# Kernel tuning notes

Measured on AMD Instinct MI355X. Metric: run time of the kernel, lower is better.

The kernel has to match this reference:

```python
import jax, jax.numpy as jnp
import numpy as np

N, E, G = 50000, 800000, 128      # nodes, edges, graphs
IN, H, OUT = 128, 128, 2          # feature dims
K, L = 3, 3                       # Chebyshev order, num conv layers
EPS = 1e-5


def setup_inputs() -> dict:
    key = jax.random.key(0)
    ks = jax.random.split(key, 10)
    x = jax.random.normal(ks[0], (N, IN), dtype=jnp.float32)
    edge_index = jax.random.randint(ks[1], (2, E), 0, N, dtype=jnp.int64)
    batch = jnp.sort(jax.random.randint(ks[2], (N,), 0, G, dtype=jnp.int64))
    w_in = jax.random.normal(ks[3], (IN, H), dtype=jnp.float32) * 0.05
    b_in = jnp.zeros((H,), jnp.float32)
    ln_g = jnp.ones((H,), jnp.float32)
    ln_b = jnp.zeros((H,), jnp.float32)
    cheb_w = jax.random.normal(ks[4], (L, K, H, H), dtype=jnp.float32) * 0.05
    cheb_b = jnp.zeros((L, H), jnp.float32)
    bn_g = jnp.ones((L, H), jnp.float32)
    bn_b = jnp.zeros((L, H), jnp.float32)
    w1 = jax.random.normal(ks[5], (H, H // 2), dtype=jnp.float32) * 0.05
    b1 = jnp.zeros((H // 2,), jnp.float32)
    w2 = jax.random.normal(ks[6], (H // 2, OUT), dtype=jnp.float32) * 0.05
    b2 = jnp.zeros((OUT,), jnp.float32)
    return dict(x=x, w_in=w_in, b_in=b_in, ln_g=ln_g, ln_b=ln_b,
                cheb_w=cheb_w, cheb_b=cheb_b, bn_g=bn_g, bn_b=bn_b,
                w1=w1, b1=b1, w2=w2, b2=b2,
                edge_index=edge_index, batch=batch)


def reference(x, w_in, b_in, ln_g, ln_b, cheb_w, cheb_b, bn_g, bn_b,
              w1, b1, w2, b2, edge_index, batch):
    src, dst = edge_index[0], edge_index[1]

    # ChebConv scaled Laplacian with lambda_max=2, sym norm:
    # L_hat = -D^{-1/2} A D^{-1/2}  (self-loop terms cancel in PyG's __norm__)
    deg = jax.ops.segment_sum(jnp.ones((E,), x.dtype), src, num_segments=N)
    dinv = jnp.where(deg > 0, jax.lax.rsqrt(jnp.maximum(deg, 1.0)), 0.0)
    w_edge = -dinv[src] * dinv[dst]  # [E]

    def spmm(h):  # y_i = sum_{(j->i)} w_edge * h_j
        return jax.ops.segment_sum(w_edge[:, None] * h[src], dst, num_segments=N)

    # node_embed: Linear -> LayerNorm -> ReLU (dropout p used in eval => identity)
    h = x @ w_in + b_in
    mu = h.mean(-1, keepdims=True)
    var = h.var(-1, keepdims=True)
    h = (h - mu) * jax.lax.rsqrt(var + EPS) * ln_g + ln_b
    h = jax.nn.relu(h)

    hiddens = [h]
    for l in range(L):
        # Chebyshev recurrence: T0 = h, T1 = L_hat h, Tk = 2 L_hat T_{k-1} - T_{k-2}
        tx0 = h
        out = tx0 @ cheb_w[l, 0]
        tx1 = spmm(tx0)
        out = out + tx1 @ cheb_w[l, 1]
        for k in range(2, K):
            tx2 = 2.0 * spmm(tx1) - tx0
            out = out + tx2 @ cheb_w[l, k]
            tx0, tx1 = tx1, tx2
        out = out + cheb_b[l]
        # BatchNorm1d over nodes (training-mode batch statistics, biased var)
        m = out.mean(0)
        v = out.var(0)
        out = (out - m) * jax.lax.rsqrt(v + EPS) * bn_g[l] + bn_b[l]
        h = jax.nn.relu(out)
        hiddens.append(h)

    # Laplacian (Dirichlet) regularization over all hidden states
    reg = jnp.float32(0.0)
    for hh in hiddens:
        diff = hh[src] - hh[dst]              # [E, H]
        reg = reg + jnp.mean(jnp.sum(diff * diff, axis=-1))
    reg = reg / len(hiddens)

    # global mean pool over batch assignment
    counts = jax.ops.segment_sum(jnp.ones((N,), x.dtype), batch, num_segments=G)
    gsum = jax.ops.segment_sum(h, batch, num_segments=G)
    gmean = gsum / jnp.maximum(counts, 1.0)[:, None]

    z = jax.nn.relu(gmean @ w1 + b1)
    logits = z @ w2 + b2
    return logits, reg
```

## Files before the change

### kernel.cpp

```cpp
#include <hip/hip_runtime.h>
#include <hip/hip_bf16.h>

#define NNODES 50000
#define NEDGES 800000
#define NGRAPH 128
#define CAP 64
#define EPSV 1e-5f

typedef __attribute__((ext_vector_type(8))) short bf16x8;
typedef __attribute__((ext_vector_type(8))) unsigned short us16x8;
typedef __attribute__((ext_vector_type(4))) float f32x4;
typedef __attribute__((ext_vector_type(2))) float f32x2;

__device__ __forceinline__ unsigned short f2bf(float f) {
    unsigned u = __float_as_uint(f);
    return (unsigned short)((u + 0x7fffu + ((u >> 16) & 1u)) >> 16);
}
__device__ __forceinline__ float bf2f(unsigned short h) {
    return __uint_as_float(((unsigned)h) << 16);
}
__device__ __forceinline__ unsigned pk4_fp8(float a, float b, float c, float d) {
    int w = __builtin_amdgcn_cvt_pk_fp8_f32(a, b, 0, false);
    w = __builtin_amdgcn_cvt_pk_fp8_f32(c, d, w, true);
    return (unsigned)w;
}

__global__ void fillA_kernel(const int* __restrict__ src, const int* __restrict__ dst,
                             int* __restrict__ outdeg, int* __restrict__ indeg,
                             unsigned* __restrict__ slot, int E) {
    int e = blockIdx.x * blockDim.x + threadIdx.x;
    if (e < E) {
        int s = src[e];
        int d = dst[e];
        atomicAdd(&outdeg[s], 1);
        int pos = atomicAdd(&indeg[d], 1);
        if (pos < CAP) slot[(size_t)d * CAP + pos] = (unsigned)s;
    }
}

__global__ void dinv_gstart_kernel(const int* __restrict__ outdeg, float* __restrict__ dinv,
                                   const int* __restrict__ batch, int* __restrict__ gstart, int n) {
    int i = blockIdx.x * blockDim.x + threadIdx.x;
    if (i < n) {
        int d = outdeg[i];
        dinv[i] = (d > 0) ? rsqrtf((float)d) : 0.0f;
    }
    if (blockIdx.x == 0 && threadIdx.x <= NGRAPH) {
        int g = threadIdx.x;
        int lo = 0, hi = n;
        while (lo < hi) {
            int mid = (lo + hi) >> 1;
            if (batch[mid] < g) lo = mid + 1; else hi = mid;
        }
        gstart[g] = lo;
    }
}

__global__ void pack_kernel(unsigned* __restrict__ slot, const int* __restrict__ indeg,
                            const float* __restrict__ dinv, int total) {
    int i = blockIdx.x * blockDim.x + threadIdx.x;
    if (i >= total) return;
    int node = i >> 6, k = i & (CAP - 1);
    int cnt = min(indeg[node], CAP);
    if (k < cnt) {
        unsigned idx = slot[i];
        slot[i] = idx | ((unsigned)f2bf(dinv[idx]) << 16);
    }
}

__global__ void wprep_kernel(const float* __restrict__ w_in, const float* __restrict__ cheb_w,
                             unsigned short* __restrict__ Wsp) {
    int p = blockIdx.x;
    int t = threadIdx.x;
    for (int s8 = 0; s8 < 8; ++s8) {
        int slot = s8 * 256 + t;
        int kc = slot >> 9, ct = (slot >> 6) & 7, lane = slot & 63;
        int q = lane >> 4, nn = lane & 15;
        unsigned short* o = Wsp + ((size_t)p * 2048 + slot) * 16;
#pragma unroll
        for (int j = 0; j < 8; ++j) {
            int k = kc * 32 + q * 8 + j, c = ct * 16 + nn;
            float v;
            if (p == 0) {
                v = w_in[k * 128 + c];
            } else {
                int pl = (p - 1) / 3, kk = (p - 1) % 3;
                v = cheb_w[((size_t)(pl * 3 + kk) * 128 + k) * 128 + c];
                if (kk == 0) v -= cheb_w[((size_t)(pl * 3 + 2) * 128 + k) * 128 + c];
                else if (kk == 2) v *= 2.f;
            }
            unsigned short hi = f2bf(v);
            o[j] = hi;
            o[8 + j] = f2bf(v - bf2f(hi));
        }
    }
}

template <int NPARTS, int EPI, int AF32>
__global__ __launch_bounds__(256) void gemm_mfma(
    const void* __restrict__ A0v, const void* __restrict__ A1v, const void* __restrict__ A2v,
    const unsigned short* __restrict__ Wsp, const float* __restrict__ bias,
    unsigned short* __restrict__ out16,
    const float* __restrict__ g0, const float* __restrict__ b0,
    float* __restrict__ colsum, float* __restrict__ colsumsq, int n) {
    __shared__ float red[256];
    int t = threadIdx.x, w = t >> 6, l = t & 63;
    int m = l & 15, qk = l >> 4;
    int rowA = blockIdx.x * 64 + w * 16 + m;
    red[t] = 0.f;
    __syncthreads();

    f32x4 acc[8];
#pragma unroll
    for (int ct = 0; ct < 8; ++ct) acc[ct] = (f32x4){0.f, 0.f, 0.f, 0.f};

    bool valid = rowA < n;
#pragma unroll
    for (int p = 0; p < NPARTS; ++p) {
#pragma unroll
        for (int kc = 0; kc < 4; ++kc) {
            bf16x8 ah, al;
            if (AF32) {
                const float* arow = (const float*)A0v;
                if (p == 1) arow = (const float*)A1v;
                if (p == 2) arow = (const float*)A2v;
                arow += (size_t)rowA * 128;
                float4 x0, x1;
                if (valid) {
                    x0 = *(const float4*)&arow[kc * 32 + qk * 8];
                    x1 = *(const float4*)&arow[kc * 32 + qk * 8 + 4];
                } else {
                    x0 = make_float4(0.f, 0.f, 0.f, 0.f); x1 = x0;
                }
                float xs[8] = {x0.x, x0.y, x0.z, x0.w, x1.x, x1.y, x1.z, x1.w};
#pragma unroll
                for (int j = 0; j < 8; ++j) {
                    unsigned short hi = f2bf(xs[j]);
                    ah[j] = (short)hi;
                    al[j] = (short)f2bf(xs[j] - bf2f(hi));
                }
            } else {
                const unsigned short* arow = (const unsigned short*)A0v;
                if (p == 1) arow = (const unsigned short*)A1v;
                if (p == 2) arow = (const unsigned short*)A2v;
                arow += (size_t)rowA * 128;
                if (valid) ah = *(const bf16x8*)&arow[kc * 32 + qk * 8];
                else ah = (bf16x8){0, 0, 0, 0, 0, 0, 0, 0};
            }
            const unsigned short* wb = Wsp + ((size_t)((p * 4 + kc) * 8) * 64 + l) * 16;
#pragma unroll
            for (int ct = 0; ct < 8; ++ct) {
                bf16x8 bh = *(const bf16x8*)(wb + (size_t)ct * 64 * 16);
                bf16x8 bl = *(const bf16x8*)(wb + (size_t)ct * 64 * 16 + 8);
                acc[ct] = __builtin_amdgcn_mfma_f32_16x16x32_bf16(ah, bh, acc[ct], 0, 0, 0);
                if (AF32)
                    acc[ct] = __builtin_amdgcn_mfma_f32_16x16x32_bf16(al, bh, acc[ct], 0, 0, 0);
                acc[ct] = __builtin_amdgcn_mfma_f32_16x16x32_bf16(ah, bl, acc[ct], 0, 0, 0);
            }
        }
    }

    int rowC0 = blockIdx.x * 64 + w * 16 + qk * 4;
    if (EPI == 0) {
        float rs[4] = {0.f, 0.f, 0.f, 0.f}, rss[4] = {0.f, 0.f, 0.f, 0.f};
#pragma unroll
        for (int ct = 0; ct < 8; ++ct) {
            float b = bias[ct * 16 + m];
#pragma unroll
            for (int j = 0; j < 4; ++j) {
                float v = acc[ct][j] + b;
                acc[ct][j] = v;
                rs[j] += v; rss[j] += v * v;
            }
        }
#pragma unroll
        for (int off = 1; off < 16; off <<= 1) {
#pragma unroll
            for (int j = 0; j < 4; ++j) {
                rs[j] += __shfl_xor(rs[j], off, 64);
                rss[j] += __shfl_xor(rss[j], off, 64);
            }
        }
        float mean[4], rstd[4];
#pragma unroll
        for (int j = 0; j < 4; ++j) {
            mean[j] = rs[j] * (1.f / 128.f);
            float var = rss[j] * (1.f / 128.f) - mean[j] * mean[j];
            rstd[j] = rsqrtf(var + EPSV);
        }
#pragma unroll
        for (int ct = 0; ct < 8; ++ct) {
            int c = ct * 16 + m;
            float gg = g0[c], bb = b0[c];
#pragma unroll
            for (int j = 0; j < 4; ++j) {
                int gr = rowC0 + j;
                if (gr < n) {
                    float x = (acc[ct][j] - mean[j]) * rstd[j] * gg + bb;
                    x = fmaxf(x, 0.f);
                    out16[(size_t)gr * 128 + c] = f2bf(x);
                }
            }
        }
    } else {
#pragma unroll
        for (int ct = 0; ct < 8; ++ct) {
            int c = ct * 16 + m;
            float b = bias[c];
            float s = 0.f, ss = 0.f;
#pragma unroll
            for (int j = 0; j < 4; ++j) {
                int gr = rowC0 + j;
                if (gr < n) {
                    float v = acc[ct][j] + b;
                    out16[(size_t)gr * 128 + c] = f2bf(v);
                    s += v; ss += v * v;
                }
            }
            s += __shfl_xor(s, 16, 64);  ss += __shfl_xor(ss, 16, 64);
            s += __shfl_xor(s, 32, 64);  ss += __shfl_xor(ss, 32, 64);
            if (qk == 0) {
                atomicAdd(&red[c], s);
                atomicAdd(&red[128 + c], ss);
            }
        }
        __syncthreads();
        if (t < 128) {
            atomicAdd(&colsum[t], red[t]);
            atomicAdd(&colsumsq[t], red[128 + t]);
        }
    }
}

__global__ void repack8_kernel(const unsigned short* __restrict__ h16,
                               unsigned char* __restrict__ h8, int total8) {
    int i = blockIdx.x * blockDim.x + threadIdx.x;
    if (i >= total8) return;
    us16x8 a = ((const us16x8*)h16)[i];
    uint2 o;
    o.x = pk4_fp8(bf2f(a[0]), bf2f(a[1]), bf2f(a[2]), bf2f(a[3]));
    o.y = pk4_fp8(bf2f(a[4]), bf2f(a[5]), bf2f(a[6]), bf2f(a[7]));
    ((uint2*)h8)[i] = o;
}

template <int MODE>
__global__ void spmm_g(const unsigned char* __restrict__ g8,
                       const unsigned short* __restrict__ self16,
                       unsigned short* __restrict__ dst16, unsigned char* __restrict__ dst8,
                       const unsigned* __restrict__ slot,
                       const float* __restrict__ dinv,
                       const int* __restrict__ outdeg, const int* __restrict__ indeg,
                       int n, double* __restrict__ norm_slots, double* __restrict__ cross_slots) {
    int lane = threadIdx.x & 63;
    int g = lane >> 4;
    int q = lane & 15;
    int w = (int)((blockIdx.x * (unsigned)blockDim.x + threadIdx.x) >> 6) * 4 + g;
    bool active = w < n;
    int cnt = active ? min(indeg[w], CAP) : 0;
    size_t rbase = (size_t)w * 128 + q * 8;
    float hi[8];
    if (MODE != 1) {
#pragma unroll
        for (int j = 0; j < 8; ++j) hi[j] = 0.f;
        if (active) {
            us16x8 a = *(const us16x8*)&self16[rbase];
#pragma unroll
            for (int j = 0; j < 8; ++j) hi[j] = bf2f(a[j]);
        }
    }
    float acc[8];
#pragma unroll
    for (int j = 0; j < 8; ++j) acc[j] = 0.f;
    float cr = 0.f;
    size_t sbase = (size_t)w * CAP;
#pragma unroll
    for (int c = 0; c < 4; ++c) {
        if (c * 16 >= cnt) break;
        unsigned cw = (c * 16 + q < cnt) ? slot[sbase + c * 16 + q] : 0u;
        int mycnt = min(cnt - c * 16, 16);
        uint2 uu[16];
        float dd[16];
#pragma unroll
        for (int u = 0; u < 16; ++u) {
            unsigned cwu = __shfl(cw, (g << 4) + u, 64);
            int j = (int)(cwu & 0xFFFFu);
            dd[u] = bf2f((unsigned short)(cwu >> 16));
            uu[u] = make_uint2(0, 0);
            if (u < mycnt) uu[u] = *(const uint2*)&g8[(size_t)j * 128 + q * 8];
        }
#pragma unroll
        for (int u = 0; u < 16; ++u) {
            f32x2 l0 = __builtin_amdgcn_cvt_pk_f32_fp8(uu[u].x, false);
            f32x2 h0 = __builtin_amdgcn_cvt_pk_f32_fp8(uu[u].x, true);
            f32x2 l1 = __builtin_amdgcn_cvt_pk_f32_fp8(uu[u].y, false);
            f32x2 h1 = __builtin_amdgcn_cvt_pk_f32_fp8(uu[u].y, true);
            float v[8] = {l0.x, l0.y, h0.x, h0.y, l1.x, l1.y, h1.x, h1.y};
            if (MODE != 2) {
#pragma unroll
                for (int j = 0; j < 8; ++j) acc[j] += dd[u] * v[j];
            }
            if (MODE != 1) {
#pragma unroll
                for (int j = 0; j < 8; ++j) cr += hi[j] * v[j];
            }
        }
    }
    if (MODE != 2 && active) {
        float di = dinv[w];
        float v[8];
        us16x8 o;
#pragma unroll
        for (int j = 0; j < 8; ++j) { v[j] = -di * acc[j]; o[j] = f2bf(v[j]); }
        *(us16x8*)&dst16[rbase] = o;
        if (MODE == 0) {
            uint2 o8;
            o8.x = pk4_fp8(v[0], v[1], v[2], v[3]);
            o8.y = pk4_fp8(v[4], v[5], v[6], v[7]);
            *(uint2*)&dst8[(size_t)w * 128 + q * 8] = o8;
        }
    }
    if (MODE != 1) {
        float nt = 0.f;
#pragma unroll
        for (int j = 0; j < 8; ++j) nt += hi[j] * hi[j];
#pragma unroll
        for (int off = 8; off > 0; off >>= 1) {
            cr += __shfl_down(cr, off, 16);
            nt += __shfl_down(nt, off, 16);
        }
        if (q == 0 && active) {
            int slotid = w & 255;
            atomicAdd(&cross_slots[slotid], (double)cr);
            atomicAdd(&norm_slots[slotid], (double)nt * (double)(outdeg[w] + indeg[w]));
        }
    }
}

__global__ void bnrelu_kernel(const unsigned short* __restrict__ ob16,
                              const float* __restrict__ colsum, const float* __restrict__ colsumsq,
                              const float* __restrict__ bn_g, const float* __restrict__ bn_b,
                              unsigned short* __restrict__ h16, unsigned char* __restrict__ h8,
                              int n, int total4) {
    __shared__ float ssc[128], ssh[128];
    int t = threadIdx.x;
    if (t < 128) {
        float m = colsum[t] / (float)n;
        float v = colsumsq[t] / (float)n - m * m;
        float sc = bn_g[t] * rsqrtf(v + EPSV);
        ssc[t] = sc;
        ssh[t] = bn_b[t] - m * sc;
    }
    __syncthreads();
    int i = blockIdx.x * blockDim.x + t;
    if (i >= total4) return;
    ushort4 o = ((const ushort4*)ob16)[i];
    int c = (i * 4) & 127;
    float4 r;
    r.x = fmaxf(bf2f(o.x) * ssc[c + 0] + ssh[c + 0], 0.f);
    r.y = fmaxf(bf2f(o.y) * ssc[c + 1] + ssh[c + 1], 0.f);
    r.z = fmaxf(bf2f(o.z) * ssc[c + 2] + ssh[c + 2], 0.f);
    r.w = fmaxf(bf2f(o.w) * ssc[c + 3] + ssh[c + 3], 0.f);
    ushort4 u = make_ushort4(f2bf(r.x), f2bf(r.y), f2bf(r.z), f2bf(r.w));
    ((ushort4*)h16)[i] = u;
    ((unsigned*)h8)[i] = pk4_fp8(r.x, r.y, r.z, r.w);
}

__global__ void poolmlp_kernel(const unsigned short* __restrict__ h16, const int* __restrict__ start,
                               const float* __restrict__ w1, const float* __restrict__ b1,
                               const float* __restrict__ w2, const float* __restrict__ b2,
                               const double* __restrict__ norm_slots,
                               const double* __restrict__ cross_slots,
                               float* __restrict__ out) {
    __shared__ float sm[2][128];
    __shared__ float gm[128];
    int g = blockIdx.x, t = threadIdx.x;
    int half = t >> 7, c = t & 127;
    int s = start[g], e = start[g + 1];
    float acc = 0.f;
    for (int r = s + half; r < e; r += 2) acc += bf2f(h16[(size_t)r * 128 + c]);
    sm[half][c] = acc;
    __syncthreads();
    if (t < 128) {
        float cnt = fmaxf((float)(e - s), 1.f);
        gm[t] = (sm[0][t] + sm[1][t]) / cnt;
    }
    __syncthreads();
    if (t < 64) {
        float z = b1[t];
        for (int k = 0; k < 128; ++k) z += gm[k] * w1[(size_t)k * 64 + t];
        z = fmaxf(z, 0.f);
        float p0 = z * w2[t * 2 + 0];
        float p1 = z * w2[t * 2 + 1];
        for (int off = 32; off > 0; off >>= 1) {
            p0 += __shfl_down(p0, off, 64);
            p1 += __shfl_down(p1, off, 64);
        }
        if (t == 0) {
            out[g * 2 + 0] = p0 + b2[0];
            out[g * 2 + 1] = p1 + b2[1];
        }
    } else if (g == 0 && t < 128) {
        int l = t - 64;
        double ns = 0.0, cs = 0.0;
        for (int i = l; i < 256; i += 64) { ns += norm_slots[i]; cs += cross_slots[i]; }
        for (int off = 32; off > 0; off >>= 1) {
            ns += __shfl_down(ns, off, 64);
            cs += __shfl_down(cs, off, 64);
        }
        if (l == 0) out[256] = (float)((ns - 2.0 * cs) / ((double)NEDGES * 4.0));
    }
}

extern "C" void kernel_launch(void* const* d_in, const int* in_sizes, int n_in,
                              void* d_out, int out_size, void* d_ws, size_t ws_size,
                              hipStream_t stream) {
    const float* x      = (const float*)d_in[0];
    const float* w_in   = (const float*)d_in[1];
    const float* b_in   = (const float*)d_in[2];
    const float* ln_g   = (const float*)d_in[3];
    const float* ln_b   = (const float*)d_in[4];
    const float* cheb_w = (const float*)d_in[5];
    const float* cheb_b = (const float*)d_in[6];
    const float* bn_g   = (const float*)d_in[7];
    const float* bn_b   = (const float*)d_in[8];
    const float* w1     = (const float*)d_in[9];
    const float* b1     = (const float*)d_in[10];
    const float* w2     = (const float*)d_in[11];
    const float* b2     = (const float*)d_in[12];
    const int*   eidx   = (const int*)d_in[13];
    const int*   batch  = (const int*)d_in[14];
    const int* src = eidx;
    const int* dst = eidx + NEDGES;
    float* out = (float*)d_out;

    char* ws = (char*)d_ws;
    size_t off = 0;
    auto alloc = [&](size_t bytes) -> void* {
        void* p = ws + off;
        off = (off + bytes + 255) & ~(size_t)255;
        return p;
    };
    unsigned short* ob16 = (unsigned short*)alloc((size_t)NNODES * 128 * 2);
    unsigned short* h16  = (unsigned short*)alloc((size_t)NNODES * 128 * 2);
    unsigned short* t116 = (unsigned short*)alloc((size_t)NNODES * 128 * 2);
    unsigned short* s16  = (unsigned short*)alloc((size_t)NNODES * 128 * 2);
    unsigned char*  h8   = (unsigned char*)alloc((size_t)NNODES * 128);
    unsigned char*  t18  = (unsigned char*)alloc((size_t)NNODES * 128);
    unsigned short* Wsp  = (unsigned short*)alloc((size_t)10 * 2048 * 16 * 2);
    int* degs     = (int*)alloc((size_t)2 * NNODES * 4);
    int* outdeg   = degs;
    int* indeg    = degs + NNODES;
    float* dinv   = (float*)alloc((size_t)NNODES * 4);
    unsigned* slot = (unsigned*)alloc((size_t)NNODES * CAP * 4);
    int* gstart   = (int*)alloc((size_t)(NGRAPH + 1) * 4);
    float* colstats = (float*)alloc(768 * 4 + 512 * 8);
    double* dslots  = (double*)(colstats + 768);
    double* norm_slots  = dslots;
    double* cross_slots = dslots + 256;

    hipMemsetAsync(degs, 0, (size_t)2 * NNODES * 4, stream);
    hipMemsetAsync(colstats, 0, 768 * 4 + 512 * 8, stream);

    int tE = (NEDGES + 255) / 256;
    int tN = (NNODES + 255) / 256;
    fillA_kernel<<<tE, 256, 0, stream>>>(src, dst, outdeg, indeg, slot, NEDGES);
    dinv_gstart_kernel<<<tN, 256, 0, stream>>>(outdeg, dinv, batch, gstart, NNODES);
    pack_kernel<<<(NNODES * CAP + 255) / 256, 256, 0, stream>>>(slot, indeg, dinv, NNODES * CAP);
    wprep_kernel<<<10, 256, 0, stream>>>(w_in, cheb_w, Wsp);

    int gemmBlocks = (NNODES + 63) / 64;
    int nodes4 = (NNODES + 3) / 4;
    int spmmBlocks = (nodes4 * 64 + 255) / 256;
    int total4 = NNODES * 128 / 4;
    int total8 = NNODES * 128 / 8;

    gemm_mfma<1, 0, 1><<<gemmBlocks, 256, 0, stream>>>(x, nullptr, nullptr, Wsp, b_in, h16,
                                                       ln_g, ln_b, nullptr, nullptr, NNODES);
    repack8_kernel<<<(total8 + 255) / 256, 256, 0, stream>>>(h16, h8, total8);

    for (int l = 0; l < 3; ++l) {
        float* colsum = colstats + 256 * l;
        float* colsumsq = colsum + 128;
        spmm_g<0><<<spmmBlocks, 256, 0, stream>>>(h8, h16, t116, t18, slot, dinv,
                                                  outdeg, indeg, NNODES, norm_slots, cross_slots);
        spmm_g<1><<<spmmBlocks, 256, 0, stream>>>(t18, nullptr, s16, nullptr, slot, dinv,
                                                  outdeg, indeg, NNODES, nullptr, nullptr);
        gemm_mfma<3, 1, 0><<<gemmBlocks, 256, 0, stream>>>(h16, t116, s16,
            Wsp + (size_t)(1 + 3 * l) * 2048 * 16, cheb_b + (size_t)l * 128, ob16,
            nullptr, nullptr, colsum, colsumsq, NNODES);
        bnrelu_kernel<<<(total4 + 255) / 256, 256, 0, stream>>>(ob16, colsum, colsumsq,
            bn_g + (size_t)l * 128, bn_b + (size_t)l * 128, h16, h8, NNODES, total4);
    }
    spmm_g<2><<<spmmBlocks, 256, 0, stream>>>(h8, h16, nullptr, nullptr, slot, dinv,
                                              outdeg, indeg, NNODES, norm_slots, cross_slots);

    poolmlp_kernel<<<NGRAPH, 256, 0, stream>>>(h16, gstart, w1, b1, w2, b2,
                                               norm_slots, cross_slots, out);
}
```

Baseline: 695.8 us.

## Stage GEMM weights in LDS with register prefetch and fold dinv kernel into pack

The MFMA GEMM now copies each part's split-bf16 weight tile into shared memory, prefetching the next part's weights into registers while computing. All A-operand rows are loaded up front instead of inside the loop. Separately, the standalone dinv/gstart kernel and its dinv buffer are removed: pack and spmm compute rsqrt(outdeg) inline, saving one launch and one array. The LDS footprint grows to 64 KB per block, which can lower occupancy, and the extra barriers plus the larger register set add cost of their own.

```diff
diff --git a/kernel.cpp b/kernel.cpp
--- a/kernel.cpp
+++ b/kernel.cpp
@@ -38,13 +38,10 @@
     }
 }
 
-__global__ void dinv_gstart_kernel(const int* __restrict__ outdeg, float* __restrict__ dinv,
-                                   const int* __restrict__ batch, int* __restrict__ gstart, int n) {
-    int i = blockIdx.x * blockDim.x + threadIdx.x;
-    if (i < n) {
-        int d = outdeg[i];
-        dinv[i] = (d > 0) ? rsqrtf((float)d) : 0.0f;
-    }
+__global__ void pack_kernel(unsigned* __restrict__ slot, const int* __restrict__ indeg,
+                            const int* __restrict__ outdeg,
+                            const int* __restrict__ batch, int* __restrict__ gstart,
+                            int total, int n) {
     if (blockIdx.x == 0 && threadIdx.x <= NGRAPH) {
         int g = threadIdx.x;
         int lo = 0, hi = n;
@@ -54,17 +51,15 @@
         }
         gstart[g] = lo;
     }
-}
-
-__global__ void pack_kernel(unsigned* __restrict__ slot, const int* __restrict__ indeg,
-                            const float* __restrict__ dinv, int total) {
     int i = blockIdx.x * blockDim.x + threadIdx.x;
     if (i >= total) return;
     int node = i >> 6, k = i & (CAP - 1);
     int cnt = min(indeg[node], CAP);
     if (k < cnt) {
         unsigned idx = slot[i];
-        slot[i] = idx | ((unsigned)f2bf(dinv[idx]) << 16);
+        int d = outdeg[idx];
+        float dv = (d > 0) ? rsqrtf((float)d) : 0.0f;
+        slot[i] = idx | ((unsigned)f2bf(dv) << 16);
     }
 }
 
@@ -103,36 +98,79 @@
     unsigned short* __restrict__ out16,
     const float* __restrict__ g0, const float* __restrict__ b0,
     float* __restrict__ colsum, float* __restrict__ colsumsq, int n) {
-    __shared__ float red[256];
+    __shared__ unsigned short lds_hi[2048 * 8];
+    __shared__ unsigned short lds_lo[2048 * 8];
     int t = threadIdx.x, w = t >> 6, l = t & 63;
     int m = l & 15, qk = l >> 4;
     int rowA = blockIdx.x * 64 + w * 16 + m;
-    red[t] = 0.f;
-    __syncthreads();
+    bool valid = rowA < n;
 
     f32x4 acc[8];
 #pragma unroll
     for (int ct = 0; ct < 8; ++ct) acc[ct] = (f32x4){0.f, 0.f, 0.f, 0.f};
 
-    bool valid = rowA < n;
+    uint4 aB[NPARTS][4];
+    float4 aF[4][2];
+    if (AF32) {
+        const float* arow = (const float*)A0v + (size_t)rowA * 128;
+#pragma unroll
+        for (int kc = 0; kc < 4; ++kc) {
+            if (valid) {
+                aF[kc][0] = *(const float4*)&arow[kc * 32 + qk * 8];
+                aF[kc][1] = *(const float4*)&arow[kc * 32 + qk * 8 + 4];
+            } else {
+                aF[kc][0] = make_float4(0.f, 0.f, 0.f, 0.f);
+                aF[kc][1] = aF[kc][0];
+            }
+        }
+    } else {
+#pragma unroll
+        for (int p = 0; p < NPARTS; ++p) {
+            const unsigned short* arow = (const unsigned short*)A0v;
+            if (p == 1) arow = (const unsigned short*)A1v;
+            if (p == 2) arow = (const unsigned short*)A2v;
+            arow += (size_t)rowA * 128;
+#pragma unroll
+            for (int kc = 0; kc < 4; ++kc) {
+                if (valid) aB[p][kc] = *(const uint4*)&arow[kc * 32 + qk * 8];
+                else aB[p][kc] = make_uint4(0, 0, 0, 0);
+            }
+        }
+    }
+
+    const uint4* gw0 = (const uint4*)Wsp;
+    uint4 wrH[8], wrL[8];
+#pragma unroll
+    for (int i = 0; i < 8; ++i) {
+        int s = t + 256 * i;
+        wrH[i] = gw0[(size_t)s * 2];
+        wrL[i] = gw0[(size_t)s * 2 + 1];
+    }
 #pragma unroll
     for (int p = 0; p < NPARTS; ++p) {
+        __syncthreads();
+#pragma unroll
+        for (int i = 0; i < 8; ++i) {
+            int s = t + 256 * i;
+            ((uint4*)lds_hi)[s] = wrH[i];
+            ((uint4*)lds_lo)[s] = wrL[i];
+        }
+        __syncthreads();
+        if (p + 1 < NPARTS) {
+            const uint4* gw = gw0 + (size_t)(p + 1) * 2048 * 2;
+#pragma unroll
+            for (int i = 0; i < 8; ++i) {
+                int s = t + 256 * i;
+                wrH[i] = gw[(size_t)s * 2];
+                wrL[i] = gw[(size_t)s * 2 + 1];
+            }
+        }
 #pragma unroll
         for (int kc = 0; kc < 4; ++kc) {
             bf16x8 ah, al;
             if (AF32) {
-                const float* arow = (const float*)A0v;
-                if (p == 1) arow = (const float*)A1v;
-                if (p == 2) arow = (const float*)A2v;
-                arow += (size_t)rowA * 128;
-                float4 x0, x1;
-                if (valid) {
-                    x0 = *(const float4*)&arow[kc * 32 + qk * 8];
-                    x1 = *(const float4*)&arow[kc * 32 + qk * 8 + 4];
-                } else {
-                    x0 = make_float4(0.f, 0.f, 0.f, 0.f); x1 = x0;
-                }
-                float xs[8] = {x0.x, x0.y, x0.z, x0.w, x1.x, x1.y, x1.z, x1.w};
+                float xs[8] = {aF[kc][0].x, aF[kc][0].y, aF[kc][0].z, aF[kc][0].w,
+                               aF[kc][1].x, aF[kc][1].y, aF[kc][1].z, aF[kc][1].w};
 #pragma unroll
                 for (int j = 0; j < 8; ++j) {
                     unsigned short hi = f2bf(xs[j]);
@@ -140,18 +178,13 @@
                     al[j] = (short)f2bf(xs[j] - bf2f(hi));
                 }
             } else {
-                const unsigned short* arow = (const unsigned short*)A0v;
-                if (p == 1) arow = (const unsigned short*)A1v;
-                if (p == 2) arow = (const unsigned short*)A2v;
-                arow += (size_t)rowA * 128;
-                if (valid) ah = *(const bf16x8*)&arow[kc * 32 + qk * 8];
-                else ah = (bf16x8){0, 0, 0, 0, 0, 0, 0, 0};
-            }
-            const unsigned short* wb = Wsp + ((size_t)((p * 4 + kc) * 8) * 64 + l) * 16;
+                ah = __builtin_bit_cast(bf16x8, aB[p][kc]);
+            }
 #pragma unroll
             for (int ct = 0; ct < 8; ++ct) {
-                bf16x8 bh = *(const bf16x8*)(wb + (size_t)ct * 64 * 16);
-                bf16x8 bl = *(const bf16x8*)(wb + (size_t)ct * 64 * 16 + 8);
+                int sl = (kc * 8 + ct) * 64 + l;
+                bf16x8 bh = *(const bf16x8*)&lds_hi[sl * 8];
+                bf16x8 bl = *(const bf16x8*)&lds_lo[sl * 8];
                 acc[ct] = __builtin_amdgcn_mfma_f32_16x16x32_bf16(ah, bh, acc[ct], 0, 0, 0);
                 if (AF32)
                     acc[ct] = __builtin_amdgcn_mfma_f32_16x16x32_bf16(al, bh, acc[ct], 0, 0, 0);
@@ -203,6 +236,10 @@
             }
         }
     } else {
+        __syncthreads();
+        float* red = (float*)lds_hi;
+        red[t] = 0.f;
+        __syncthreads();
 #pragma unroll
         for (int ct = 0; ct < 8; ++ct) {
             int c = ct * 16 + m;
@@ -248,7 +285,6 @@
                        const unsigned short* __restrict__ self16,
                        unsigned short* __restrict__ dst16, unsigned char* __restrict__ dst8,
                        const unsigned* __restrict__ slot,
-                       const float* __restrict__ dinv,
                        const int* __restrict__ outdeg, const int* __restrict__ indeg,
                        int n, double* __restrict__ norm_slots, double* __restrict__ cross_slots) {
     int lane = threadIdx.x & 63;
@@ -257,6 +293,8 @@
     int w = (int)((blockIdx.x * (unsigned)blockDim.x + threadIdx.x) >> 6) * 4 + g;
     bool active = w < n;
     int cnt = active ? min(indeg[w], CAP) : 0;
+    int od = active ? outdeg[w] : 0;
+    float di = (od > 0) ? rsqrtf((float)od) : 0.f;
     size_t rbase = (size_t)w * 128 + q * 8;
     float hi[8];
     if (MODE != 1) {
@@ -306,7 +344,6 @@
         }
     }
     if (MODE != 2 && active) {
-        float di = dinv[w];
         float v[8];
         us16x8 o;
 #pragma unroll
@@ -331,7 +368,7 @@
         if (q == 0 && active) {
             int slotid = w & 255;
             atomicAdd(&cross_slots[slotid], (double)cr);
-            atomicAdd(&norm_slots[slotid], (double)nt * (double)(outdeg[w] + indeg[w]));
+            atomicAdd(&norm_slots[slotid], (double)nt * (double)(od + indeg[w]));
         }
     }
 }
@@ -450,7 +487,6 @@
     int* degs     = (int*)alloc((size_t)2 * NNODES * 4);
     int* outdeg   = degs;
     int* indeg    = degs + NNODES;
-    float* dinv   = (float*)alloc((size_t)NNODES * 4);
     unsigned* slot = (unsigned*)alloc((size_t)NNODES * CAP * 4);
     int* gstart   = (int*)alloc((size_t)(NGRAPH + 1) * 4);
     float* colstats = (float*)alloc(768 * 4 + 512 * 8);
@@ -462,10 +498,10 @@
     hipMemsetAsync(colstats, 0, 768 * 4 + 512 * 8, stream);
 
     int tE = (NEDGES + 255) / 256;
-    int tN = (NNODES + 255) / 256;
     fillA_kernel<<<tE, 256, 0, stream>>>(src, dst, outdeg, indeg, slot, NEDGES);
-    dinv_gstart_kernel<<<tN, 256, 0, stream>>>(outdeg, dinv, batch, gstart, NNODES);
-    pack_kernel<<<(NNODES * CAP + 255) / 256, 256, 0, stream>>>(slot, indeg, dinv, NNODES * CAP);
+    pack_kernel<<<(NNODES * CAP + 255) / 256, 256, 0, stream>>>(slot, indeg, outdeg,
+                                                                batch, gstart,
+                                                                NNODES * CAP, NNODES);
     wprep_kernel<<<10, 256, 0, stream>>>(w_in, cheb_w, Wsp);
 
     int gemmBlocks = (NNODES + 63) / 64;
@@ -481,9 +517,9 @@
     for (int l = 0; l < 3; ++l) {
         float* colsum = colstats + 256 * l;
         float* colsumsq = colsum + 128;
-        spmm_g<0><<<spmmBlocks, 256, 0, stream>>>(h8, h16, t116, t18, slot, dinv,
+        spmm_g<0><<<spmmBlocks, 256, 0, stream>>>(h8, h16, t116, t18, slot,
                                                   outdeg, indeg, NNODES, norm_slots, cross_slots);
-        spmm_g<1><<<spmmBlocks, 256, 0, stream>>>(t18, nullptr, s16, nullptr, slot, dinv,
+        spmm_g<1><<<spmmBlocks, 256, 0, stream>>>(t18, nullptr, s16, nullptr, slot,
                                                   outdeg, indeg, NNODES, nullptr, nullptr);
         gemm_mfma<3, 1, 0><<<gemmBlocks, 256, 0, stream>>>(h16, t116, s16,
             Wsp + (size_t)(1 + 3 * l) * 2048 * 16, cheb_b + (size_t)l * 128, ob16,
@@ -491,7 +527,7 @@
         bnrelu_kernel<<<(total4 + 255) / 256, 256, 0, stream>>>(ob16, colsum, colsumsq,
             bn_g + (size_t)l * 128, bn_b + (size_t)l * 128, h16, h8, NNODES, total4);
     }
-    spmm_g<2><<<spmmBlocks, 256, 0, stream>>>(h8, h16, nullptr, nullptr, slot, dinv,
+    spmm_g<2><<<spmmBlocks, 256, 0, stream>>>(h8, h16, nullptr, nullptr, slot,
                                               outdeg, indeg, NNODES, norm_slots, cross_slots);
 
     poolmlp_kernel<<<NGRAPH, 256, 0, stream>>>(h16, gstart, w1, b1, w2, b2,
```

New measurement: 792.9 us. 14.0% more time.
